# Optimization experiments

Measured on AMD Instinct MI355X. Metric: run time of the kernel, lower is better.

## Reference

```python
import jax, jax.numpy as jnp
import numpy as np

EPS = 1e-5  # BatchNorm2d default eps


def _bn(x, gamma, beta, mean, var):
    # inference-mode BN over channel dim (NCHW)
    inv = gamma / jnp.sqrt(var + EPS)
    return x * inv[None, :, None, None] + (beta - mean * inv)[None, :, None, None]


def _shift(x):
    # 4 channel groups shifted by 1 pixel in 4 directions, zero-fill at borders
    C = x.shape[1]
    gc = C // 4
    g0, g1, g2, g3 = (x[:, i * gc:(i + 1) * gc] for i in range(4))
    g0 = jnp.pad(g0[:, :, :, :-1], ((0, 0), (0, 0), (0, 0), (1, 0)))  # shift right (W)
    g1 = jnp.pad(g1[:, :, 1:, :], ((0, 0), (0, 0), (0, 1), (0, 0)))   # shift up (H)
    g2 = jnp.pad(g2[:, :, :, 1:], ((0, 0), (0, 0), (0, 0), (0, 1)))   # shift left (W)
    g3 = jnp.pad(g3[:, :, :-1, :], ((0, 0), (0, 0), (1, 0), (0, 0)))  # shift down (H)
    return jnp.concatenate([g0, g1, g2, g3], axis=1)


def setup_inputs() -> dict:
    key = jax.random.key(0)
    ks = jax.random.split(key, 8)
    B, C1, C2, H, W = 16, 128, 256, 128, 128
    x = jax.random.normal(ks[0], (B, C1, H, W), dtype=jnp.float32)
    w_conv = jax.random.normal(ks[1], (C2, C1, 3, 3), dtype=jnp.float32) * (1.0 / np.sqrt(C1 * 9))
    w_1x1 = jax.random.normal(ks[2], (C2, C2, 1, 1), dtype=jnp.float32) * (1.0 / np.sqrt(C2))
    b_1x1 = jax.random.normal(ks[3], (C2,), dtype=jnp.float32) * 0.05
    gamma = jax.random.uniform(ks[4], (C2,), dtype=jnp.float32, minval=0.5, maxval=1.5)
    beta = jax.random.normal(ks[5], (C2,), dtype=jnp.float32) * 0.1
    bn_mean = jax.random.normal(ks[6], (C2,), dtype=jnp.float32) * 0.1
    bn_var = jax.random.uniform(ks[7], (C2,), dtype=jnp.float32, minval=0.5, maxval=1.5)
    return {"x": x, "w_conv": w_conv, "w_1x1": w_1x1, "b_1x1": b_1x1,
            "gamma": gamma, "beta": beta, "bn_mean": bn_mean, "bn_var": bn_var}


def reference(x, w_conv, w_1x1, b_1x1, gamma, beta, bn_mean, bn_var):
    # conv3x3 (stride 1, 'same' via autopad=1, no bias) + BN + SiLU
    y = jax.lax.conv_general_dilated(
        x, w_conv, window_strides=(1, 1), padding=((1, 1), (1, 1)),
        dimension_numbers=("NCHW", "OIHW", "NCHW"))
    y = jax.nn.silu(_bn(y, gamma, beta, bn_mean, bn_var))
    identity = y
    # shift + conv1x1 (with bias) + same BN + residual + SiLU
    z = _shift(y)
    z = jax.lax.conv_general_dilated(
        z, w_1x1, window_strides=(1, 1), padding=((0, 0), (0, 0)),
        dimension_numbers=("NCHW", "OIHW", "NCHW")) + b_1x1[None, :, None, None]
    z = _bn(z, gamma, beta, bn_mean, bn_var) + identity
    return jax.nn.silu(z)
```

## Files before the change

kernel.cpp:

```cpp
#include <hip/hip_runtime.h>

typedef unsigned short u16;
typedef unsigned int   u32;
typedef __bf16 bf16x8 __attribute__((ext_vector_type(8)));
typedef float  f32x4  __attribute__((ext_vector_type(4)));

__device__ __forceinline__ float bf2f(u16 v){ u32 u = ((u32)v) << 16; float f; __builtin_memcpy(&f,&u,4); return f; }
__device__ __forceinline__ u16 f2bf(float f){ u32 u; __builtin_memcpy(&u,&f,4); u32 r = (u + 0x7FFFu + ((u>>16)&1u)) >> 16; return (u16)r; }
__device__ __forceinline__ float silu(float v){ return v / (1.f + __expf(-v)); }

__device__ __forceinline__ void gload_lds16(const u16* g, u16* l){
  __builtin_amdgcn_global_load_lds((const __attribute__((address_space(1))) void*)g,
                                   (__attribute__((address_space(3))) void*)l, 16, 0, 0);
}

#define FENCE asm volatile("" ::: "memory")
#define BARRIER do{ FENCE; __builtin_amdgcn_s_barrier(); FENCE; }while(0)

#define HP 130
#define XPIX 128
#define YPIX 256
#define XIMG (HP*HP*XPIX)
#define YIMG (HP*HP*YPIX)

__global__ void prep_coef(const float* __restrict__ gamma, const float* __restrict__ beta,
                          const float* __restrict__ mean,  const float* __restrict__ var,
                          const float* __restrict__ b1, float2* __restrict__ coefA, float2* __restrict__ coefB){
  int c = threadIdx.x;
  float s = gamma[c] * rsqrtf(var[c] + 1e-5f);
  float t = beta[c] - mean[c] * s;
  coefA[c] = make_float2(s, t);
  coefB[c] = make_float2(s, b1[c] * s + t);
}

__global__ void repack_w3(const float* __restrict__ w, u16* __restrict__ w3p){
  int idx = blockIdx.x*256 + threadIdx.x;
  int n = idx / 1152, k = idx % 1152;
  int tap = k >> 7, c = k & 127;
  int kh = tap / 3, kw = tap % 3;
  w3p[idx] = f2bf(w[((n*128 + c)*3 + kh)*3 + kw]);
}

__global__ void repack_w1(const float* __restrict__ w, u16* __restrict__ w1p){
  int idx = blockIdx.x*256 + threadIdx.x;
  w1p[idx] = f2bf(w[idx]);
}

__device__ __forceinline__ void halo_pix(int pi, int& hp, int& wp){
  if (pi < 130){ hp = 0; wp = pi; }
  else if (pi < 260){ hp = 129; wp = pi - 130; }
  else { int j = pi - 260; hp = 1 + (j >> 1); wp = (j & 1) ? 129 : 0; }
}
__global__ void zero_halos(u16* __restrict__ xpad, u16* __restrict__ ypad, int cimg){
  int idx = blockIdx.x*256 + threadIdx.x;
  const int NX = cimg*516*16;
  uint4 z = make_uint4(0u,0u,0u,0u);
  if (idx < NX){
    int b = idx / (516*16), rr = idx % (516*16);
    int pi = rr >> 4, cch = rr & 15, hp, wp;
    halo_pix(pi, hp, wp);
    *(uint4*)(xpad + (((size_t)b*HP + hp)*HP + wp)*XPIX + cch*8) = z;
  } else {
    idx -= NX;
    if (idx < cimg*516*32){
      int b = idx / (516*32), rr = idx % (516*32);
      int pi = rr >> 5, cch = rr & 31, hp, wp;
      halo_pix(pi, hp, wp);
      *(uint4*)(ypad + (((size_t)b*HP + hp)*HP + wp)*YPIX + cch*8) = z;
    }
  }
}

__global__ __launch_bounds__(256) void transpose_x(const float* __restrict__ x, u16* __restrict__ xpad, int b0){
  __shared__ u16 s[128][130];
  const int tid = threadIdx.x;
  const int bl = blockIdx.x >> 7, h = blockIdx.x & 127;
  const int lane = tid & 63, wv = tid >> 6;
  const float2* src = (const float2*)(x + ((size_t)(b0 + bl)*128)*16384 + (size_t)h*128);
  #pragma unroll
  for (int it = 0; it < 32; ++it){
    const int c = it*4 + wv;
    float2 v = src[(size_t)c*8192 + lane];
    s[c][2*lane]   = f2bf(v.x);
    s[c][2*lane+1] = f2bf(v.y);
  }
  __syncthreads();
  u16* dst = xpad + (((size_t)bl*HP + h + 1)*HP + 1)*XPIX;
  #pragma unroll
  for (int it = 0; it < 32; ++it){
    const int w = it*4 + wv;
    u32 v = (u32)s[2*lane][w] | ((u32)s[2*lane+1][w] << 16);
    *(u32*)(dst + (size_t)w*XPIX + 2*lane) = v;
  }
}


__device__ __forceinline__ int offA_of(int Ts){
  int tap = Ts >> 1;
  int kh = (tap*11) >> 5;
  int kw = tap - kh*3;
  return kh*(HP*XPIX) + kw*XPIX + ((Ts & 1) << 6);
}

__global__ __launch_bounds__(512, 2) void convA(const u16* __restrict__ xpad, const u16* __restrict__ w3p,
                                                const float2* __restrict__ coefA, u16* __restrict__ ypad,
                                                int BPW){
  __shared__ u16 sA[2][16384];
  __shared__ u16 sB[2][16384];
  const int t = threadIdx.x;
  const int nwg = gridDim.x;
  const int w = (blockIdx.x & 7)*(nwg >> 3) + (blockIdx.x >> 3);
  const int band0 = w * BPW;
  const int bl = band0 >> 6;
  int h0 = (band0 & 63) << 1;
  const int lane = t & 63, wave = t >> 6;
  const int wm = wave & 1, wn = wave >> 1;
  const int quad = lane >> 4, l16 = lane & 15;
  const int lc = t & 7;
  const u16* ximg = xpad + (size_t)bl * XIMG;

  const u16* gA[2][2]; int lA[2][2];
  const u16* gB[2][2]; int lB[2][2];
  #pragma unroll
  for (int ho = 0; ho < 2; ++ho)
    #pragma unroll
    for (int q = 0; q < 2; ++q){
      int r = ((t >> 6) << 4) + (q << 3) + ((t >> 3) & 7);
      int p = (ho << 6) + r + (r & 64);
      gA[ho][q] = ximg + (size_t)((h0 + (p >> 7))*HP + (p & 127))*XPIX + ((lc ^ (p & 7)) << 3);
      lA[ho][q] = p*64 + lc*8;
      int n = ((r >> 5) << 6) + (ho << 5) + (r & 31);
      gB[ho][q] = w3p + (size_t)n*1152 + ((lc ^ (n & 7)) << 3);
      lB[ho][q] = n*64 + lc*8;
    }

  u32 fA[2][4][2], fB[4][2];
  #pragma unroll
  for (int hf = 0; hf < 2; ++hf)
    #pragma unroll
    for (int i = 0; i < 4; ++i)
      #pragma unroll
      for (int c = 0; c < 2; ++c){
        int row = wm*128 + hf*64 + i*16 + l16;
        fA[hf][i][c] = row*64 + (((c*4 + quad) ^ (row & 7)) << 3);
      }
  #pragma unroll
  for (int j = 0; j < 4; ++j)
    #pragma unroll
    for (int c = 0; c < 2; ++c){
      int row = wn*64 + j*16 + l16;
      fB[j][c] = row*64 + (((c*4 + quad) ^ (row & 7)) << 3);
    }

  f32x4 acc[8][4];
  #pragma unroll
  for (int i = 0; i < 8; ++i)
    #pragma unroll
    for (int j = 0; j < 4; ++j){ f32x4 z = {0.f,0.f,0.f,0.f}; acc[i][j] = z; }

  {
    gload_lds16(gA[0][0], sA[0] + lA[0][0]); gload_lds16(gA[0][1], sA[0] + lA[0][1]);
    gload_lds16(gB[0][0], sB[0] + lB[0][0]); gload_lds16(gB[0][1], sB[0] + lB[0][1]);
    gload_lds16(gB[1][0], sB[0] + lB[1][0]); gload_lds16(gB[1][1], sB[0] + lB[1][1]);
    gload_lds16(gA[1][0], sA[0] + lA[1][0]); gload_lds16(gA[1][1], sA[0] + lA[1][1]);
    asm volatile("s_waitcnt vmcnt(0)" ::: "memory");
  }
  BARRIER;

  const int UTOT = 18 * BPW;
  int tn = 0;
  for (int u = 0; u < UTOT; ++u){
    const int pr = u & 1;
    const u16* A = sA[pr]; const u16* B = sB[pr];
    u16* An = sA[pr ^ 1]; u16* Bn = sB[pr ^ 1];
    const bool last = (u == UTOT - 1);
    const int ntl = (tn == 17) ? 0 : tn + 1;
    if (tn == 17 && !last){
      #pragma unroll
      for (int ho = 0; ho < 2; ++ho)
        #pragma unroll
        for (int q = 0; q < 2; ++q) gA[ho][q] += 2*HP*XPIX;
    }
    const int aoff = offA_of(ntl), boff = ntl*64;

    bf16x8 a[4][2], b[4][2];
    #pragma unroll
    for (int i = 0; i < 4; ++i){
      a[i][0] = *(const bf16x8*)(A + fA[0][i][0]);
      a[i][1] = *(const bf16x8*)(A + fA[0][i][1]);
    }
    #pragma unroll
    for (int j = 0; j < 4; ++j){
      b[j][0] = *(const bf16x8*)(B + fB[j][0]);
      b[j][1] = *(const bf16x8*)(B + fB[j][1]);
    }
    if (!last){
      gload_lds16(gA[0][0] + aoff, An + lA[0][0]); gload_lds16(gA[0][1] + aoff, An + lA[0][1]);
      gload_lds16(gB[0][0] + boff, Bn + lB[0][0]); gload_lds16(gB[0][1] + boff, Bn + lB[0][1]);
    }
    __builtin_amdgcn_s_setprio(1);
    #pragma unroll
    for (int i = 0; i < 4; ++i)
      #pragma unroll
      for (int j = 0; j < 4; ++j){
        acc[i][j] = __builtin_amdgcn_mfma_f32_16x16x32_bf16(a[i][0], b[j][0], acc[i][j], 0, 0, 0);
        acc[i][j] = __builtin_amdgcn_mfma_f32_16x16x32_bf16(a[i][1], b[j][1], acc[i][j], 0, 0, 0);
      }
    __builtin_amdgcn_s_setprio(0);
    if (last) asm volatile("s_waitcnt vmcnt(0)" ::: "memory");
    else      asm volatile("s_waitcnt vmcnt(4)" ::: "memory");
    BARRIER;

    #pragma unroll
    for (int i = 0; i < 4; ++i){
      a[i][0] = *(const bf16x8*)(A + fA[1][i][0]);
      a[i][1] = *(const bf16x8*)(A + fA[1][i][1]);
    }
    if (!last){
      gload_lds16(gB[1][0] + boff, Bn + lB[1][0]); gload_lds16(gB[1][1] + boff, Bn + lB[1][1]);
      gload_lds16(gA[1][0] + aoff, An + lA[1][0]); gload_lds16(gA[1][1] + aoff, An + lA[1][1]);
    }
    __builtin_amdgcn_s_setprio(1);
    #pragma unroll
    for (int i = 0; i < 4; ++i)
      #pragma unroll
      for (int j = 0; j < 4; ++j){
        acc[4+i][j] = __builtin_amdgcn_mfma_f32_16x16x32_bf16(a[i][0], b[j][0], acc[4+i][j], 0, 0, 0);
        acc[4+i][j] = __builtin_amdgcn_mfma_f32_16x16x32_bf16(a[i][1], b[j][1], acc[4+i][j], 0, 0, 0);
      }
    __builtin_amdgcn_s_setprio(0);
    if (!last) asm volatile("s_waitcnt vmcnt(2)" ::: "memory");
    BARRIER;

    if (tn == 17){
      float2 co[4];
      #pragma unroll
      for (int j = 0; j < 4; ++j) co[j] = coefA[wn*64 + j*16 + l16];
      #pragma unroll
      for (int ig = 0; ig < 8; ++ig){
        const int pb = wm*128 + ig*16 + quad*4;
        #pragma unroll
        for (int r = 0; r < 4; ++r){
          const int p = pb + r;
          const int hh = h0 + (p >> 7), ww = p & 127;
          u16* dst = ypad + ((size_t)(bl*HP + hh + 1)*HP + (ww + 1))*YPIX + wn*64;
          #pragma unroll
          for (int j = 0; j < 4; ++j){
            float v = acc[ig][j][r]*co[j].x + co[j].y;
            dst[j*16 + l16] = f2bf(silu(v));
          }
        }
      }
      asm volatile("s_waitcnt vmcnt(0)" ::: "memory");
      h0 += 2;
      tn = 0;
      #pragma unroll
      for (int i = 0; i < 8; ++i)
        #pragma unroll
        for (int j = 0; j < 4; ++j){ f32x4 z = {0.f,0.f,0.f,0.f}; acc[i][j] = z; }
    } else ++tn;
  }
}

__global__ __launch_bounds__(256, 2) void convB(const u16* __restrict__ ypad, const u16* __restrict__ w1p,
                                                const float2* __restrict__ coefB, float* __restrict__ out, int b0){
  __shared__ u16 sAct[2][8192];
  __shared__ u16 sW[2][8192];
  const int tid = threadIdx.x;
  const int nwg = gridDim.x;
  const int bidl = (blockIdx.x & 7)*(nwg >> 3) + (blockIdx.x >> 3);
  const int nt = bidl & 1, row = bidl >> 1;
  const int bl = row >> 7, h = row & 127;
  const int n0 = nt << 7;
  const int lane = tid & 63, wave = tid >> 6;
  const int wc = wave & 1, wpx = wave >> 1;
  const int quad = lane >> 4, l16 = lane & 15;

  const size_t imgy = (size_t)bl * YIMG;

  const u16* gact[4]; const u16* gwt[4]; int ldst[4];
  #pragma unroll
  for (int l = 0; l < 4; ++l){
    int id = l*256 + tid;
    int p = id >> 3, c = id & 7;
    gact[l] = ypad + imgy + (size_t)(h*HP)*YPIX + (size_t)p*YPIX + ((c ^ (p & 7)) << 3);
    gwt[l]  = w1p + (size_t)(n0 + p)*256 + ((c ^ (p & 7)) << 3);
    ldst[l] = id*8;
  }

  u32 fW[4][2], fAc[4][2];
  #pragma unroll
  for (int i = 0; i < 4; ++i)
    #pragma unroll
    for (int k = 0; k < 2; ++k){
      int rn = wc*64 + i*16 + l16;
      fW[i][k] = rn*64 + (((k*4 + quad) ^ (rn & 7)) << 3);
      int rp = wpx*64 + i*16 + l16;
      fAc[i][k] = rp*64 + (((k*4 + quad) ^ (rp & 7)) << 3);
    }

  f32x4 acc[4][4];
  #pragma unroll
  for (int i = 0; i < 4; ++i)
    #pragma unroll
    for (int j = 0; j < 4; ++j){ f32x4 zz = {0.f,0.f,0.f,0.f}; acc[i][j] = zz; }

  {
    const int aoff = (1*HP + 0)*YPIX + 0;
    #pragma unroll
    for (int l = 0; l < 4; ++l){
      gload_lds16(gact[l] + aoff, sAct[0] + ldst[l]);
      gload_lds16(gwt[l],         sW[0]   + ldst[l]);
    }
    asm volatile("s_waitcnt vmcnt(0)" ::: "memory");
  }
  BARRIER;

  #pragma unroll
  for (int g = 0; g < 4; ++g){
    const int pr = g & 1;
    if (g < 3){
      const int gg = g + 1;
      const int dhp = (gg == 1) ? 2 : ((gg == 3) ? 0 : 1);
      const int dwp = (gg == 0) ? 0 : ((gg == 2) ? 2 : 1);
      const int aoff = (dhp*HP + dwp)*YPIX + gg*64;
      const int woff = gg*64;
      #pragma unroll
      for (int l = 0; l < 4; ++l){
        gload_lds16(gact[l] + aoff, sAct[pr^1] + ldst[l]);
        gload_lds16(gwt[l] + woff,  sW[pr^1]   + ldst[l]);
      }
    }
    bf16x8 wf[4][2], af[4][2];
    #pragma unroll
    for (int i = 0; i < 4; ++i){
      wf[i][0] = *(const bf16x8*)(sW[pr] + fW[i][0]);
      wf[i][1] = *(const bf16x8*)(sW[pr] + fW[i][1]);
      af[i][0] = *(const bf16x8*)(sAct[pr] + fAc[i][0]);
      af[i][1] = *(const bf16x8*)(sAct[pr] + fAc[i][1]);
    }
    __builtin_amdgcn_s_setprio(1);
    #pragma unroll
    for (int i = 0; i < 4; ++i)
      #pragma unroll
      for (int j = 0; j < 4; ++j){
        acc[i][j] = __builtin_amdgcn_mfma_f32_16x16x32_bf16(wf[i][0], af[j][0], acc[i][j], 0, 0, 0);
        acc[i][j] = __builtin_amdgcn_mfma_f32_16x16x32_bf16(wf[i][1], af[j][1], acc[i][j], 0, 0, 0);
      }
    __builtin_amdgcn_s_setprio(0);
    asm volatile("s_waitcnt vmcnt(0)" ::: "memory");
    BARRIER;
  }

  const size_t ybase = ((size_t)(bl*HP + h + 1))*HP*YPIX;
  const size_t obase = (size_t)(b0 + bl)*256*16384 + (size_t)h*128;
  #pragma unroll
  for (int i = 0; i < 4; ++i){
    const int chb = n0 + wc*64 + i*16 + quad*4;
    const float2 c0 = coefB[chb+0], c1 = coefB[chb+1], c2 = coefB[chb+2], c3 = coefB[chb+3];
    float* ob = out + obase + (size_t)chb*16384;
    #pragma unroll
    for (int j = 0; j < 4; ++j){
      const int p = wpx*64 + j*16 + l16;
      const ushort4 rv = *(const ushort4*)&ypad[ybase + (size_t)(p + 1)*YPIX + chb];
      ob[p]             = silu(acc[i][j][0]*c0.x + c0.y + bf2f(rv.x));
      ob[16384 + p]     = silu(acc[i][j][1]*c1.x + c1.y + bf2f(rv.y));
      ob[2*16384 + p]   = silu(acc[i][j][2]*c2.x + c2.y + bf2f(rv.z));
      ob[3*16384 + p]   = silu(acc[i][j][3]*c3.x + c3.y + bf2f(rv.w));
    }
  }
}

extern "C" void kernel_launch(void* const* d_in, const int* in_sizes, int n_in,
                              void* d_out, int out_size, void* d_ws, size_t ws_size,
                              hipStream_t stream){
  const float* x  = (const float*)d_in[0];
  const float* w3 = (const float*)d_in[1];
  const float* w1 = (const float*)d_in[2];
  const float* b1 = (const float*)d_in[3];
  const float* gm = (const float*)d_in[4];
  const float* bt = (const float*)d_in[5];
  const float* mn = (const float*)d_in[6];
  const float* vr = (const float*)d_in[7];
  float* outp = (float*)d_out;

  char* ws = (char*)d_ws;
  float2* coefA = (float2*)ws;
  float2* coefB = coefA + 256;
  u16*    w3p   = (u16*)(ws + 4096);
  u16*    w1p   = (u16*)(ws + 4096 + 589824);
  const size_t fixed = 4096 + 589824 + 131072;
  int cimg = 16;
  while (cimg > 1 && fixed + (size_t)cimg*12979200ull > ws_size) cimg >>= 1;
  u16* xpad = (u16*)(ws + fixed);
  u16* ypad = (u16*)(ws + fixed + (size_t)cimg*4326400ull);

  prep_coef<<<1, 256, 0, stream>>>(gm, bt, mn, vr, b1, coefA, coefB);
  repack_w3<<<1152, 256, 0, stream>>>(w3, w3p);
  repack_w1<<<256, 256, 0, stream>>>(w1, w1p);
  {
    int nthr = cimg*516*48;
    zero_halos<<<(nthr + 255)/256, 256, 0, stream>>>(xpad, ypad, cimg);
  }
  const int bands = 64*cimg;
  const int BPW = (bands >= 1024) ? 4 : (bands >= 512 ? 2 : 1);
  const int nwgA = bands / BPW;
  for (int b0 = 0; b0 < 16; b0 += cimg){
    transpose_x<<<128*cimg, 256, 0, stream>>>(x, xpad, b0);
    convA<<<nwgA, 512, 0, stream>>>(xpad, w3p, coefA, ypad, BPW);
    convB<<<2*128*cimg, 256, 0, stream>>>(ypad, w1p, coefB, outp, b0);
  }
}
```

Baseline: 651.4 us.

## Restructure conv3x3 main loop into register double-buffered ping-pong pipeline

Rewrites the conv3x3 GEMM main loop to process two K-steps per iteration, with full-tile LDS staging prefetched one step ahead and LDS-to-register fragment loads for the next step issued before the MFMAs of the current step. The intent is to hide LDS read latency and global-load latency behind matrix work. The cost is doubled fragment registers (aF0/aF1, bF0/bF1), which may cause spills at two waves per SIMD. It also drops the s_setprio hints and waits on vmcnt(0) at each barrier, which may add stalls.

```diff
diff --git a/kernel.cpp b/kernel.cpp
--- a/kernel.cpp
+++ b/kernel.cpp
@@ -158,107 +158,91 @@
     #pragma unroll
     for (int j = 0; j < 4; ++j){ f32x4 z = {0.f,0.f,0.f,0.f}; acc[i][j] = z; }
 
-  {
-    gload_lds16(gA[0][0], sA[0] + lA[0][0]); gload_lds16(gA[0][1], sA[0] + lA[0][1]);
-    gload_lds16(gB[0][0], sB[0] + lB[0][0]); gload_lds16(gB[0][1], sB[0] + lB[0][1]);
-    gload_lds16(gB[1][0], sB[0] + lB[1][0]); gload_lds16(gB[1][1], sB[0] + lB[1][1]);
-    gload_lds16(gA[1][0], sA[0] + lA[1][0]); gload_lds16(gA[1][1], sA[0] + lA[1][1]);
-    asm volatile("s_waitcnt vmcnt(0)" ::: "memory");
-  }
+  bf16x8 aF0[8][2], bF0[4][2], aF1[8][2], bF1[4][2];
+
+  auto STAGE = [&](int ut, u16* Ad, u16* Bd){
+    const int tb = ut % 18;
+    const int aoff = offA_of(tb), boff = tb*64;
+    gload_lds16(gA[0][0] + aoff, Ad + lA[0][0]); gload_lds16(gA[0][1] + aoff, Ad + lA[0][1]);
+    gload_lds16(gA[1][0] + aoff, Ad + lA[1][0]); gload_lds16(gA[1][1] + aoff, Ad + lA[1][1]);
+    gload_lds16(gB[0][0] + boff, Bd + lB[0][0]); gload_lds16(gB[0][1] + boff, Bd + lB[0][1]);
+    gload_lds16(gB[1][0] + boff, Bd + lB[1][0]); gload_lds16(gB[1][1] + boff, Bd + lB[1][1]);
+  };
+  auto DSR = [&](bf16x8 (&af)[8][2], bf16x8 (&bf)[4][2], const u16* Ab, const u16* Bb){
+    #pragma unroll
+    for (int hf = 0; hf < 2; ++hf)
+      #pragma unroll
+      for (int i = 0; i < 4; ++i){
+        af[hf*4+i][0] = *(const bf16x8*)(Ab + fA[hf][i][0]);
+        af[hf*4+i][1] = *(const bf16x8*)(Ab + fA[hf][i][1]);
+      }
+    #pragma unroll
+    for (int j = 0; j < 4; ++j){
+      bf[j][0] = *(const bf16x8*)(Bb + fB[j][0]);
+      bf[j][1] = *(const bf16x8*)(Bb + fB[j][1]);
+    }
+  };
+  auto MMA = [&](const bf16x8 (&af)[8][2], const bf16x8 (&bf)[4][2]){
+    #pragma unroll
+    for (int i = 0; i < 8; ++i)
+      #pragma unroll
+      for (int j = 0; j < 4; ++j){
+        acc[i][j] = __builtin_amdgcn_mfma_f32_16x16x32_bf16(af[i][0], bf[j][0], acc[i][j], 0, 0, 0);
+        acc[i][j] = __builtin_amdgcn_mfma_f32_16x16x32_bf16(af[i][1], bf[j][1], acc[i][j], 0, 0, 0);
+      }
+  };
+  auto EPI = [&](){
+    float2 co[4];
+    #pragma unroll
+    for (int j = 0; j < 4; ++j) co[j] = coefA[wn*64 + j*16 + l16];
+    #pragma unroll
+    for (int ig = 0; ig < 8; ++ig){
+      const int pb = wm*128 + ig*16 + quad*4;
+      #pragma unroll
+      for (int r = 0; r < 4; ++r){
+        const int p = pb + r;
+        const int hh = h0 + (p >> 7), ww = p & 127;
+        u16* dst = ypad + ((size_t)(bl*HP + hh + 1)*HP + (ww + 1))*YPIX + wn*64;
+        #pragma unroll
+        for (int j = 0; j < 4; ++j){
+          float v = acc[ig][j][r]*co[j].x + co[j].y;
+          dst[j*16 + l16] = f2bf(silu(v));
+        }
+      }
+    }
+    h0 += 2;
+    #pragma unroll
+    for (int i = 0; i < 8; ++i)
+      #pragma unroll
+      for (int j = 0; j < 4; ++j){ f32x4 z = {0.f,0.f,0.f,0.f}; acc[i][j] = z; }
+  };
+
+  STAGE(0, sA[0], sB[0]);
+  STAGE(1, sA[1], sB[1]);
+  asm volatile("s_waitcnt vmcnt(8)" ::: "memory");
   BARRIER;
+  DSR(aF0, bF0, sA[0], sB[0]);
 
   const int UTOT = 18 * BPW;
-  int tn = 0;
-  for (int u = 0; u < UTOT; ++u){
-    const int pr = u & 1;
-    const u16* A = sA[pr]; const u16* B = sB[pr];
-    u16* An = sA[pr ^ 1]; u16* Bn = sB[pr ^ 1];
-    const bool last = (u == UTOT - 1);
-    const int ntl = (tn == 17) ? 0 : tn + 1;
-    if (tn == 17 && !last){
+  for (int u = 0; u < UTOT; u += 2){
+    asm volatile("s_waitcnt vmcnt(0) lgkmcnt(0)" ::: "memory");
+    BARRIER;
+    if ((u % 18) == 16){
       #pragma unroll
       for (int ho = 0; ho < 2; ++ho)
         #pragma unroll
         for (int q = 0; q < 2; ++q) gA[ho][q] += 2*HP*XPIX;
     }
-    const int aoff = offA_of(ntl), boff = ntl*64;
-
-    bf16x8 a[4][2], b[4][2];
-    #pragma unroll
-    for (int i = 0; i < 4; ++i){
-      a[i][0] = *(const bf16x8*)(A + fA[0][i][0]);
-      a[i][1] = *(const bf16x8*)(A + fA[0][i][1]);
-    }
-    #pragma unroll
-    for (int j = 0; j < 4; ++j){
-      b[j][0] = *(const bf16x8*)(B + fB[j][0]);
-      b[j][1] = *(const bf16x8*)(B + fB[j][1]);
-    }
-    if (!last){
-      gload_lds16(gA[0][0] + aoff, An + lA[0][0]); gload_lds16(gA[0][1] + aoff, An + lA[0][1]);
-      gload_lds16(gB[0][0] + boff, Bn + lB[0][0]); gload_lds16(gB[0][1] + boff, Bn + lB[0][1]);
-    }
-    __builtin_amdgcn_s_setprio(1);
-    #pragma unroll
-    for (int i = 0; i < 4; ++i)
-      #pragma unroll
-      for (int j = 0; j < 4; ++j){
-        acc[i][j] = __builtin_amdgcn_mfma_f32_16x16x32_bf16(a[i][0], b[j][0], acc[i][j], 0, 0, 0);
-        acc[i][j] = __builtin_amdgcn_mfma_f32_16x16x32_bf16(a[i][1], b[j][1], acc[i][j], 0, 0, 0);
-      }
-    __builtin_amdgcn_s_setprio(0);
-    if (last) asm volatile("s_waitcnt vmcnt(0)" ::: "memory");
-    else      asm volatile("s_waitcnt vmcnt(4)" ::: "memory");
+    if (u + 2 < UTOT) STAGE(u + 2, sA[0], sB[0]);
+    DSR(aF1, bF1, sA[1], sB[1]);
+    MMA(aF0, bF0);
+
+    asm volatile("s_waitcnt vmcnt(0) lgkmcnt(0)" ::: "memory");
     BARRIER;
-
-    #pragma unroll
-    for (int i = 0; i < 4; ++i){
-      a[i][0] = *(const bf16x8*)(A + fA[1][i][0]);
-      a[i][1] = *(const bf16x8*)(A + fA[1][i][1]);
-    }
-    if (!last){
-      gload_lds16(gB[1][0] + boff, Bn + lB[1][0]); gload_lds16(gB[1][1] + boff, Bn + lB[1][1]);
-      gload_lds16(gA[1][0] + aoff, An + lA[1][0]); gload_lds16(gA[1][1] + aoff, An + lA[1][1]);
-    }
-    __builtin_amdgcn_s_setprio(1);
-    #pragma unroll
-    for (int i = 0; i < 4; ++i)
-      #pragma unroll
-      for (int j = 0; j < 4; ++j){
-        acc[4+i][j] = __builtin_amdgcn_mfma_f32_16x16x32_bf16(a[i][0], b[j][0], acc[4+i][j], 0, 0, 0);
-        acc[4+i][j] = __builtin_amdgcn_mfma_f32_16x16x32_bf16(a[i][1], b[j][1], acc[4+i][j], 0, 0, 0);
-      }
-    __builtin_amdgcn_s_setprio(0);
-    if (!last) asm volatile("s_waitcnt vmcnt(2)" ::: "memory");
-    BARRIER;
-
-    if (tn == 17){
-      float2 co[4];
-      #pragma unroll
-      for (int j = 0; j < 4; ++j) co[j] = coefA[wn*64 + j*16 + l16];
-      #pragma unroll
-      for (int ig = 0; ig < 8; ++ig){
-        const int pb = wm*128 + ig*16 + quad*4;
-        #pragma unroll
-        for (int r = 0; r < 4; ++r){
-          const int p = pb + r;
-          const int hh = h0 + (p >> 7), ww = p & 127;
-          u16* dst = ypad + ((size_t)(bl*HP + hh + 1)*HP + (ww + 1))*YPIX + wn*64;
-          #pragma unroll
-          for (int j = 0; j < 4; ++j){
-            float v = acc[ig][j][r]*co[j].x + co[j].y;
-            dst[j*16 + l16] = f2bf(silu(v));
-          }
-        }
-      }
-      asm volatile("s_waitcnt vmcnt(0)" ::: "memory");
-      h0 += 2;
-      tn = 0;
-      #pragma unroll
-      for (int i = 0; i < 8; ++i)
-        #pragma unroll
-        for (int j = 0; j < 4; ++j){ f32x4 z = {0.f,0.f,0.f,0.f}; acc[i][j] = z; }
-    } else ++tn;
+    if (u + 3 < UTOT) STAGE(u + 3, sA[1], sB[1]);
+    if (u + 2 < UTOT) DSR(aF0, bF0, sA[0], sB[0]);
+    MMA(aF1, bF1);
+    if ((u % 18) == 16) EPI();
   }
 }
 
```

Measured after the change: 1.371 ms. +110.6%, slower.
